# Kernel optimization log

Measured on AMD Instinct MI355X. Metric: run time of the kernel, lower is better.

Reference implementation:

```python
import jax, jax.numpy as jnp
import numpy as np

NUM_HEADS = 12
D = 768
HD = D // NUM_HEADS  # 64

def setup_inputs() -> dict:
    key = jax.random.key(0)
    ks = jax.random.split(key, 9)
    s = 0.02
    return {
        "x": jax.random.normal(ks[0], (4, 2048, D), dtype=jnp.float32),
        "QW_w": jax.random.normal(ks[1], (D, D), dtype=jnp.float32) * s,
        "QW_b": jax.random.normal(ks[2], (D,), dtype=jnp.float32) * s,
        "KW_w": jax.random.normal(ks[3], (D, D), dtype=jnp.float32) * s,
        "KW_b": jax.random.normal(ks[4], (D,), dtype=jnp.float32) * s,
        "VW_w": jax.random.normal(ks[5], (D, D), dtype=jnp.float32) * s,
        "VW_b": jax.random.normal(ks[6], (D,), dtype=jnp.float32) * s,
        "OW_w": jax.random.normal(ks[7], (D, D), dtype=jnp.float32) * s,
        "OW_b": jax.random.normal(ks[8], (D,), dtype=jnp.float32) * s,
    }

def reference(x, QW_w, QW_b, KW_w, KW_b, VW_w, VW_b, OW_w, OW_b):
    b, s, _ = x.shape
    # torch nn.Linear: y = x @ W.T + b
    def proj(w, bias):
        y = jnp.einsum('bsd,ed->bse', x, w) + bias
        return y.reshape(b, s, NUM_HEADS, HD).transpose(0, 2, 1, 3)  # [b,h,s,hd]
    q = proj(QW_w, QW_b)
    k = proj(KW_w, KW_b)
    v = proj(VW_w, VW_b)
    scores = jnp.einsum('bhqd,bhkd->bhqk', q, k) / jnp.sqrt(jnp.float32(HD))
    attn = jax.nn.softmax(scores, axis=-1)
    out = jnp.einsum('bhqk,bhkd->bhqd', attn, v)
    out = out.transpose(0, 2, 1, 3).reshape(b, s, NUM_HEADS * HD)
    return jnp.einsum('bsd,ed->bse', out, OW_w) + OW_b
```

## Files before the change

kernel.cpp:

```cpp
#include <hip/hip_runtime.h>
#include <hip/hip_bf16.h>

#define NH  12
#define HD  64
#define DIM 768
#define SEQ 2048
#define NB  4
#define MM  (NB*SEQ)
#define NKB (SEQ/64)

typedef short    v8s  __attribute__((ext_vector_type(8)));
typedef float    v4f  __attribute__((ext_vector_type(4)));
typedef float    v16f __attribute__((ext_vector_type(16)));
typedef unsigned v4u  __attribute__((ext_vector_type(4)));

#if __has_builtin(__builtin_amdgcn_exp2f)
#define EXP2(x) __builtin_amdgcn_exp2f(x)
#else
#define EXP2(x) __builtin_exp2f(x)
#endif

static __device__ __forceinline__ unsigned short f2b(float f) {
    unsigned int u = __float_as_uint(f);
    return (unsigned short)((u + 0x7FFFu + ((u >> 16) & 1u)) >> 16);
}
static __device__ __forceinline__ unsigned pk2bf(float lo, float hi) {
    return __builtin_amdgcn_perm(__float_as_uint(hi) + 0x8000u,
                                 __float_as_uint(lo) + 0x8000u, 0x07060302u);
}
static __device__ __forceinline__ void g2l16(const unsigned short* g, unsigned short* l) {
    __builtin_amdgcn_global_load_lds(
        (const __attribute__((address_space(1))) void*)g,
        (__attribute__((address_space(3))) void*)l, 16, 0, 0);
}

__global__ void cast_f32_bf16(const float* __restrict__ in,
                              unsigned short* __restrict__ out, int n4) {
    int i = blockIdx.x * blockDim.x + threadIdx.x;
    if (i < n4) {
        float4 v = reinterpret_cast<const float4*>(in)[i];
        ushort4 o;
        o.x = f2b(v.x); o.y = f2b(v.y); o.z = f2b(v.z); o.w = f2b(v.w);
        reinterpret_cast<ushort4*>(out)[i] = o;
    }
}

__global__ void cast4_f32_bf16(const float* __restrict__ i0, const float* __restrict__ i1,
                               const float* __restrict__ i2, const float* __restrict__ i3,
                               unsigned short* __restrict__ o0, unsigned short* __restrict__ o1,
                               unsigned short* __restrict__ o2, unsigned short* __restrict__ o3,
                               int n4) {
    int i = blockIdx.x * blockDim.x + threadIdx.x;
    if (i >= n4) return;
    const float* in; unsigned short* out;
    switch (blockIdx.y) {
        case 0: in = i0; out = o0; break;
        case 1: in = i1; out = o1; break;
        case 2: in = i2; out = o2; break;
        default: in = i3; out = o3; break;
    }
    float4 v = reinterpret_cast<const float4*>(in)[i];
    ushort4 o;
    o.x = f2b(v.x); o.y = f2b(v.y); o.z = f2b(v.z); o.w = f2b(v.w);
    reinterpret_cast<ushort4*>(out)[i] = o;
}

__global__ __launch_bounds__(256, 3) void gemm_qkv(
    const unsigned short* __restrict__ A,
    const unsigned short* __restrict__ Wq,
    const unsigned short* __restrict__ Wk,
    const unsigned short* __restrict__ Wv,
    const float* __restrict__ bq,
    const float* __restrict__ bk,
    const float* __restrict__ bvp,
    unsigned short* __restrict__ Qb,
    unsigned short* __restrict__ Kb,
    unsigned short* __restrict__ Vf)
{
    __shared__ __align__(16) unsigned short As[128 * 64];
    __shared__ __align__(16) unsigned short Bs[3][64 * 64];

    const int tid  = threadIdx.x;
    const int w    = tid >> 6, lane = tid & 63;
    const int quad = lane >> 4, l16 = lane & 15;
    const int wm   = w & 1,  wn = w >> 1;
    const int lane8 = lane >> 3, sc = lane & 7;
    const int m0   = blockIdx.x * 128;
    const int h    = blockIdx.y;
    const int n0   = h * 64;

    v4f acc[3][4][2];
    #pragma unroll
    for (int s = 0; s < 3; ++s)
        #pragma unroll
        for (int i = 0; i < 4; ++i)
            #pragma unroll
            for (int j = 0; j < 2; ++j)
                acc[s][i][j] = v4f{0.f, 0.f, 0.f, 0.f};

    for (int kb = 0; kb < DIM; kb += 64) {
        __syncthreads();
        #pragma unroll
        for (int t = 0; t < 4; ++t) {
            int r8 = w * 32 + t * 8;
            int r  = r8 + lane8;
            int gch = sc ^ (r & 7);
            g2l16(&A[(size_t)(m0 + r) * DIM + kb + gch * 8], &As[r8 * 64]);
        }
        #pragma unroll
        for (int u = 0; u < 6; ++u) {
            int G = w * 6 + u;
            int set = G >> 3, rg = G & 7;
            int row = rg * 8 + lane8;
            int gch = sc ^ (row & 7);
            const unsigned short* Wp = (set == 0) ? Wq : (set == 1) ? Wk : Wv;
            g2l16(&Wp[(size_t)(n0 + row) * DIM + kb + gch * 8], &Bs[set][rg * 8 * 64]);
        }
        __syncthreads();
        #pragma unroll
        for (int kk = 0; kk < 64; kk += 32) {
            int chb = kk >> 3;
            v8s a[4];
            #pragma unroll
            for (int i = 0; i < 4; ++i) {
                int m = wm * 64 + i * 16 + l16;
                a[i] = *reinterpret_cast<const v8s*>(
                    &As[m * 64 + (((chb + quad) ^ (m & 7)) << 3)]);
            }
            #pragma unroll
            for (int s = 0; s < 3; ++s) {
                v8s b[2];
                #pragma unroll
                for (int j = 0; j < 2; ++j) {
                    int n = wn * 32 + j * 16 + l16;
                    b[j] = *reinterpret_cast<const v8s*>(
                        &Bs[s][n * 64 + (((chb + quad) ^ (n & 7)) << 3)]);
                }
                #pragma unroll
                for (int i = 0; i < 4; ++i)
                    #pragma unroll
                    for (int j = 0; j < 2; ++j)
                        acc[s][i][j] = __builtin_amdgcn_mfma_f32_16x16x32_bf16(
                            a[i], b[j], acc[s][i][j], 0, 0, 0);
            }
        }
    }

    #pragma unroll
    for (int s = 0; s < 2; ++s) {
        unsigned short* out = s ? Kb : Qb;
        const float* bias   = s ? bk : bq;
        const float scale   = s ? 1.0f : 0.1803368801f;
        #pragma unroll
        for (int i = 0; i < 4; ++i) {
            #pragma unroll
            for (int j = 0; j < 2; ++j) {
                int hd = wn * 32 + j * 16 + l16;
                float bias_v = bias[n0 + hd];
                #pragma unroll
                for (int r = 0; r < 4; ++r) {
                    int gm = m0 + wm * 64 + i * 16 + quad * 4 + r;
                    int bb = gm >> 11, sq = gm & (SEQ - 1);
                    out[((size_t)(bb * NH + h) * SEQ + sq) * HD + hd] =
                        f2b((acc[s][i][j][r] + bias_v) * scale);
                }
            }
        }
    }
    #pragma unroll
    for (int i = 0; i < 4; ++i) {
        #pragma unroll
        for (int j = 0; j < 2; ++j) {
            int hd = wn * 32 + j * 16 + l16;
            int hb = hd >> 5, l31v = hd & 31;
            float bias_v = bvp[n0 + hd];
            int gm0 = m0 + wm * 64 + i * 16 + quad * 4;
            int bb = gm0 >> 11, sk = gm0 & (SEQ - 1);
            int kbi = sk >> 6;
            int halfv = quad >> 1, j0 = (quad & 1) * 4;
            ushort4 pkv;
            pkv.x = f2b(acc[2][i][j][0] + bias_v);
            pkv.y = f2b(acc[2][i][j][1] + bias_v);
            pkv.z = f2b(acc[2][i][j][2] + bias_v);
            pkv.w = f2b(acc[2][i][j][3] + bias_v);
            size_t frag = ((size_t)(bb * NH + h) * NKB + kbi) * 8 + hb * 4 + i;
            *reinterpret_cast<ushort4*>(
                &Vf[frag * 512 + (halfv * 32 + l31v) * 8 + j0]) = pkv;
        }
    }
}

__global__ __launch_bounds__(256, 3) void gemm_o(
    const unsigned short* __restrict__ A,
    const unsigned short* __restrict__ W,
    const float* __restrict__ bias,
    float* __restrict__ out)
{
    __shared__ __align__(16) unsigned short As[128 * 64];
    __shared__ __align__(16) unsigned short Bs[64 * 64];

    const int tid  = threadIdx.x;
    const int w    = tid >> 6, lane = tid & 63;
    const int quad = lane >> 4, l16 = lane & 15;
    const int wm   = w & 1,  wn = w >> 1;
    const int lane8 = lane >> 3, sc = lane & 7;
    const int m0  = blockIdx.x * 128;
    const int n0l = blockIdx.y * 64;

    v4f acc[4][2];
    #pragma unroll
    for (int i = 0; i < 4; ++i)
        #pragma unroll
        for (int j = 0; j < 2; ++j)
            acc[i][j] = v4f{0.f, 0.f, 0.f, 0.f};

    for (int kb = 0; kb < DIM; kb += 64) {
        __syncthreads();
        #pragma unroll
        for (int t = 0; t < 4; ++t) {
            int r8 = w * 32 + t * 8;
            int r  = r8 + lane8;
            int gch = sc ^ (r & 7);
            g2l16(&A[(size_t)(m0 + r) * DIM + kb + gch * 8], &As[r8 * 64]);
        }
        #pragma unroll
        for (int t = 0; t < 2; ++t) {
            int r8 = (w * 2 + t) * 8;
            int r  = r8 + lane8;
            int gch = sc ^ (r & 7);
            g2l16(&W[(size_t)(n0l + r) * DIM + kb + gch * 8], &Bs[r8 * 64]);
        }
        __syncthreads();
        #pragma unroll
        for (int kk = 0; kk < 64; kk += 32) {
            v8s a[4], b[2];
            int chb = kk >> 3;
            #pragma unroll
            for (int i = 0; i < 4; ++i) {
                int m = wm * 64 + i * 16 + l16;
                a[i] = *reinterpret_cast<const v8s*>(
                    &As[m * 64 + (((chb + quad) ^ (m & 7)) << 3)]);
            }
            #pragma unroll
            for (int j = 0; j < 2; ++j) {
                int n = wn * 32 + j * 16 + l16;
                b[j] = *reinterpret_cast<const v8s*>(
                    &Bs[n * 64 + (((chb + quad) ^ (n & 7)) << 3)]);
            }
            #pragma unroll
            for (int i = 0; i < 4; ++i)
                #pragma unroll
                for (int j = 0; j < 2; ++j)
                    acc[i][j] = __builtin_amdgcn_mfma_f32_16x16x32_bf16(a[i], b[j], acc[i][j], 0, 0, 0);
        }
    }

    #pragma unroll
    for (int i = 0; i < 4; ++i) {
        #pragma unroll
        for (int j = 0; j < 2; ++j) {
            int gn = n0l + wn * 32 + j * 16 + l16;
            float bias_v = bias[gn];
            #pragma unroll
            for (int r = 0; r < 4; ++r) {
                int gm = m0 + wm * 64 + i * 16 + quad * 4 + r;
                out[(size_t)gm * DIM + gn] = acc[i][j][r] + bias_v;
            }
        }
    }
}

__global__ __launch_bounds__(256, 3) void attn(
    const unsigned short* __restrict__ Q,
    const unsigned short* __restrict__ K,
    const unsigned short* __restrict__ Vf,
    unsigned short* __restrict__ ctx)
{
    __shared__ __align__(16) unsigned short Ks[2][64 * 64];

    const int tid  = threadIdx.x;
    const int w    = tid >> 6, lane = tid & 63;
    const int l31  = lane & 31, half = lane >> 5;
    const int lane8 = lane >> 3, sc = lane & 7;
    const int bh   = blockIdx.y;
    const int b    = bh / NH, h = bh % NH;
    const int q0   = blockIdx.x * 128 + w * 32;

    const unsigned short* Qp = Q  + ((size_t)bh * SEQ + q0) * HD;
    const unsigned short* Kp = K  + (size_t)bh * SEQ * HD;
    const unsigned short* Vh = Vf + (size_t)bh * NKB * 8 * 512 + lane * 8;

    v8s bq[4];
    #pragma unroll
    for (int c = 0; c < 4; ++c)
        bq[c] = *reinterpret_cast<const v8s*>(&Qp[l31 * HD + c * 16 + half * 8]);

    v8s va[2][4];
    #pragma unroll
    for (int hb = 0; hb < 2; ++hb)
        #pragma unroll
        for (int c = 0; c < 4; ++c)
            va[hb][c] = *reinterpret_cast<const v8s*>(&Vh[(hb * 4 + c) * 512]);

    v16f o0, o1, Z;
    #pragma unroll
    for (int i = 0; i < 16; ++i) { o0[i] = 0.f; o1[i] = 0.f; Z[i] = 0.f; }
    float li = 0.f;

    const int rx = l31 & 7;
    int rdoff[4];
    #pragma unroll
    for (int c = 0; c < 4; ++c)
        rdoff[c] = l31 * 64 + (((c * 2 + half) ^ rx) << 3);

    #define STAGE_K(kb_, buf_)                                                       \
        do {                                                                         \
            _Pragma("unroll")                                                        \
            for (int t = 0; t < 2; ++t) {                                            \
                int r8  = (t * 4 + w) * 8;                                           \
                int row = r8 + lane8;                                                \
                int gch = sc ^ (row & 7);                                            \
                g2l16(&Kp[(size_t)((kb_) + row) * HD + gch * 8], &Ks[buf_][r8 * 64]);\
            }                                                                        \
        } while (0)

    STAGE_K(0, 0);

    for (int it = 0; it < NKB; ++it) {
        const int buf = it & 1;
        __syncthreads();
        if (it + 1 < NKB) STAGE_K((it + 1) * 64, buf ^ 1);

        v16f s0, s1;
        {
            v8s ka00 = *reinterpret_cast<const v8s*>(&Ks[buf][rdoff[0]]);
            v8s ka10 = *reinterpret_cast<const v8s*>(&Ks[buf][rdoff[0] + 2048]);
            s0 = __builtin_amdgcn_mfma_f32_32x32x16_bf16(ka00, bq[0], Z, 0, 0, 0);
            s1 = __builtin_amdgcn_mfma_f32_32x32x16_bf16(ka10, bq[0], Z, 0, 0, 0);
            #pragma unroll
            for (int c = 1; c < 4; ++c) {
                v8s k0 = *reinterpret_cast<const v8s*>(&Ks[buf][rdoff[c]]);
                v8s k1 = *reinterpret_cast<const v8s*>(&Ks[buf][rdoff[c] + 2048]);
                s0 = __builtin_amdgcn_mfma_f32_32x32x16_bf16(k0, bq[c], s0, 0, 0, 0);
                s1 = __builtin_amdgcn_mfma_f32_32x32x16_bf16(k1, bq[c], s1, 0, 0, 0);
            }
        }

        unsigned pk[8][2];
        #pragma unroll
        for (int g = 0; g < 4; ++g) {
            float e0 = EXP2(s0[4*g+0]), e1 = EXP2(s0[4*g+1]);
            float e2 = EXP2(s0[4*g+2]), e3 = EXP2(s0[4*g+3]);
            li += (e0 + e1) + (e2 + e3);
            pk[g][0] = pk2bf(e0, e1);
            pk[g][1] = pk2bf(e2, e3);
            float f0 = EXP2(s1[4*g+0]), f1 = EXP2(s1[4*g+1]);
            float f2 = EXP2(s1[4*g+2]), f3 = EXP2(s1[4*g+3]);
            li += (f0 + f1) + (f2 + f3);
            pk[4+g][0] = pk2bf(f0, f1);
            pk[4+g][1] = pk2bf(f2, f3);
        }

        #pragma unroll
        for (int cp = 0; cp < 4; ++cp) {
            unsigned a0 = pk[2*cp][0],   a1 = pk[2*cp][1];
            unsigned b0 = pk[2*cp+1][0], b1 = pk[2*cp+1][1];
            unsigned u0 = half ? a0 : b0;
            unsigned u1 = half ? a1 : b1;
            unsigned x0 = __shfl_xor(u0, 32);
            unsigned x1 = __shfl_xor(u1, 32);
            v4u fw;
            fw.x = half ? x0 : a0;
            fw.y = half ? x1 : a1;
            fw.z = half ? b0 : x0;
            fw.w = half ? b1 : x1;
            v8s pf = __builtin_bit_cast(v8s, fw);
            o0 = __builtin_amdgcn_mfma_f32_32x32x16_bf16(va[0][cp], pf, o0, 0, 0, 0);
            o1 = __builtin_amdgcn_mfma_f32_32x32x16_bf16(va[1][cp], pf, o1, 0, 0, 0);
        }

        if (it + 1 < NKB) {
            const unsigned short* Vn = Vh + (size_t)(it + 1) * 8 * 512;
            #pragma unroll
            for (int hb = 0; hb < 2; ++hb)
                #pragma unroll
                for (int c = 0; c < 4; ++c)
                    va[hb][c] = *reinterpret_cast<const v8s*>(&Vn[(hb * 4 + c) * 512]);
        }
    }
    #undef STAGE_K

    float inv = 1.0f / (li + __shfl_xor(li, 32));

    const int q = q0 + l31;
    size_t base = ((size_t)(b * SEQ + q)) * DIM + h * HD;
    #pragma unroll
    for (int g = 0; g < 4; ++g) {
        int hd0 = 8 * g + 4 * half;
        uint2 u0, u1;
        u0.x = pk2bf(o0[4*g+0] * inv, o0[4*g+1] * inv);
        u0.y = pk2bf(o0[4*g+2] * inv, o0[4*g+3] * inv);
        u1.x = pk2bf(o1[4*g+0] * inv, o1[4*g+1] * inv);
        u1.y = pk2bf(o1[4*g+2] * inv, o1[4*g+3] * inv);
        *reinterpret_cast<uint2*>(&ctx[base + hd0])      = u0;
        *reinterpret_cast<uint2*>(&ctx[base + 32 + hd0]) = u1;
    }
}

extern "C" void kernel_launch(void* const* d_in, const int* in_sizes, int n_in,
                              void* d_out, int out_size, void* d_ws, size_t ws_size,
                              hipStream_t stream) {
    const float* x  = (const float*)d_in[0];
    const float* qw = (const float*)d_in[1]; const float* qb = (const float*)d_in[2];
    const float* kw = (const float*)d_in[3]; const float* kb = (const float*)d_in[4];
    const float* vw = (const float*)d_in[5]; const float* vb = (const float*)d_in[6];
    const float* ow = (const float*)d_in[7]; const float* ob = (const float*)d_in[8];
    float* out = (float*)d_out;

    char* ws = (char*)d_ws;
    size_t off = 0;
    auto alloc = [&](size_t bytes) -> unsigned short* {
        unsigned short* p = (unsigned short*)(ws + off);
        off += (bytes + 255) & ~(size_t)255;
        return p;
    };
    const size_t XB = (size_t)MM * DIM * 2;
    const size_t WB = (size_t)DIM * DIM * 2;
    const size_t QB = (size_t)NB * NH * SEQ * HD * 2;

    unsigned short* xb  = alloc(XB);
    unsigned short* wqb = alloc(WB);
    unsigned short* wkb = alloc(WB);
    unsigned short* wvb = alloc(WB);
    unsigned short* wob = alloc(WB);
    unsigned short* Qb  = alloc(QB);
    unsigned short* Kb  = alloc(QB);
    unsigned short* Vfb = alloc(QB);
    unsigned short* ctx = alloc(XB);

    const int n4x = MM * DIM / 4;
    const int n4w = DIM * DIM / 4;
    cast_f32_bf16<<<(n4x + 255) / 256, 256, 0, stream>>>(x, xb, n4x);
    cast4_f32_bf16<<<dim3((n4w + 255) / 256, 4), 256, 0, stream>>>(
        qw, kw, vw, ow, wqb, wkb, wvb, wob, n4w);

    gemm_qkv<<<dim3(MM / 128, NH), 256, 0, stream>>>(
        xb, wqb, wkb, wvb, qb, kb, vb, Qb, Kb, Vfb);

    attn<<<dim3(SEQ / 128, NB * NH), 256, 0, stream>>>(Qb, Kb, Vfb, ctx);

    gemm_o<<<dim3(MM / 128, DIM / 64), 256, 0, stream>>>(ctx, wob, ob, out);
}
```

Before: 208.7 us.

## Split attention key range across two wave groups and merge cast kernels

The attention kernel now launches 512 threads per block, with two groups of four waves each processing half of the key sequence for the same 128 queries. After the loop, group 1 writes its partial outputs and row sums to shared memory, and group 0 adds them, normalizes and stores. Because the kernel uses no running max, the two partial sums can simply be added. This doubles the waves per block and halves the serial key loop, at the cost of extra LDS traffic and a block-wide reduction. Separately, the x cast and the weight cast are fused into one launch to save kernel launch overhead.

```diff
diff --git a/kernel.cpp b/kernel.cpp
--- a/kernel.cpp
+++ b/kernel.cpp
@@ -8,6 +8,7 @@
 #define NB  4
 #define MM  (NB*SEQ)
 #define NKB (SEQ/64)
+#define NKB2 (NKB/2)
 
 typedef short    v8s  __attribute__((ext_vector_type(8)));
 typedef float    v4f  __attribute__((ext_vector_type(4)));
@@ -34,35 +35,28 @@
         (__attribute__((address_space(3))) void*)l, 16, 0, 0);
 }
 
-__global__ void cast_f32_bf16(const float* __restrict__ in,
-                              unsigned short* __restrict__ out, int n4) {
+__global__ void cast_all(const float* __restrict__ x,
+                         const float* __restrict__ qw, const float* __restrict__ kw,
+                         const float* __restrict__ vw, const float* __restrict__ ow,
+                         unsigned short* __restrict__ xb,
+                         unsigned short* __restrict__ wqb, unsigned short* __restrict__ wkb,
+                         unsigned short* __restrict__ wvb, unsigned short* __restrict__ wob) {
+    const int n4x = MM * DIM / 4, n4w = DIM * DIM / 4;
     int i = blockIdx.x * blockDim.x + threadIdx.x;
-    if (i < n4) {
-        float4 v = reinterpret_cast<const float4*>(in)[i];
-        ushort4 o;
-        o.x = f2b(v.x); o.y = f2b(v.y); o.z = f2b(v.z); o.w = f2b(v.w);
-        reinterpret_cast<ushort4*>(out)[i] = o;
-    }
-}
-
-__global__ void cast4_f32_bf16(const float* __restrict__ i0, const float* __restrict__ i1,
-                               const float* __restrict__ i2, const float* __restrict__ i3,
-                               unsigned short* __restrict__ o0, unsigned short* __restrict__ o1,
-                               unsigned short* __restrict__ o2, unsigned short* __restrict__ o3,
-                               int n4) {
-    int i = blockIdx.x * blockDim.x + threadIdx.x;
-    if (i >= n4) return;
-    const float* in; unsigned short* out;
-    switch (blockIdx.y) {
-        case 0: in = i0; out = o0; break;
-        case 1: in = i1; out = o1; break;
-        case 2: in = i2; out = o2; break;
-        default: in = i3; out = o3; break;
-    }
-    float4 v = reinterpret_cast<const float4*>(in)[i];
+    if (i >= n4x + 4 * n4w) return;
+    const float* in; unsigned short* out; int idx;
+    if (i < n4x) { in = x; out = xb; idx = i; }
+    else {
+        int j = i - n4x;
+        int s = j / n4w;
+        idx = j - s * n4w;
+        in  = (s == 0) ? qw : (s == 1) ? kw : (s == 2) ? vw : ow;
+        out = (s == 0) ? wqb : (s == 1) ? wkb : (s == 2) ? wvb : wob;
+    }
+    float4 v = reinterpret_cast<const float4*>(in)[idx];
     ushort4 o;
     o.x = f2b(v.x); o.y = f2b(v.y); o.z = f2b(v.z); o.w = f2b(v.w);
-    reinterpret_cast<ushort4*>(out)[i] = o;
+    reinterpret_cast<ushort4*>(out)[idx] = o;
 }
 
 __global__ __launch_bounds__(256, 3) void gemm_qkv(
@@ -270,21 +264,25 @@
     }
 }
 
-__global__ __launch_bounds__(256, 3) void attn(
+__global__ __launch_bounds__(512, 6) void attn(
     const unsigned short* __restrict__ Q,
     const unsigned short* __restrict__ K,
     const unsigned short* __restrict__ Vf,
     unsigned short* __restrict__ ctx)
 {
-    __shared__ __align__(16) unsigned short Ks[2][64 * 64];
+    __shared__ __align__(16) unsigned short Ks[2][2][64 * 64];
+    __shared__ float Ls[4][64];
 
     const int tid  = threadIdx.x;
     const int w    = tid >> 6, lane = tid & 63;
+    const int grp  = w >> 2, wl = w & 3;
     const int l31  = lane & 31, half = lane >> 5;
     const int lane8 = lane >> 3, sc = lane & 7;
     const int bh   = blockIdx.y;
     const int b    = bh / NH, h = bh % NH;
-    const int q0   = blockIdx.x * 128 + w * 32;
+    const int q0   = blockIdx.x * 128 + wl * 32;
+    const int kbase = grp * (SEQ / 2);
+    const int kbg   = grp * NKB2;
 
     const unsigned short* Qp = Q  + ((size_t)bh * SEQ + q0) * HD;
     const unsigned short* Kp = K  + (size_t)bh * SEQ * HD;
@@ -300,7 +298,8 @@
     for (int hb = 0; hb < 2; ++hb)
         #pragma unroll
         for (int c = 0; c < 4; ++c)
-            va[hb][c] = *reinterpret_cast<const v8s*>(&Vh[(hb * 4 + c) * 512]);
+            va[hb][c] = *reinterpret_cast<const v8s*>(
+                &Vh[(size_t)kbg * 4096 + (hb * 4 + c) * 512]);
 
     v16f o0, o1, Z;
     #pragma unroll
@@ -313,34 +312,36 @@
     for (int c = 0; c < 4; ++c)
         rdoff[c] = l31 * 64 + (((c * 2 + half) ^ rx) << 3);
 
-    #define STAGE_K(kb_, buf_)                                                       \
-        do {                                                                         \
-            _Pragma("unroll")                                                        \
-            for (int t = 0; t < 2; ++t) {                                            \
-                int r8  = (t * 4 + w) * 8;                                           \
-                int row = r8 + lane8;                                                \
-                int gch = sc ^ (row & 7);                                            \
-                g2l16(&Kp[(size_t)((kb_) + row) * HD + gch * 8], &Ks[buf_][r8 * 64]);\
-            }                                                                        \
+    #define STAGE_K(kb_, buf_)                                                        \
+        do {                                                                          \
+            _Pragma("unroll")                                                         \
+            for (int t = 0; t < 2; ++t) {                                             \
+                int r8  = (t * 4 + wl) * 8;                                           \
+                int row = r8 + lane8;                                                 \
+                int gch = sc ^ (row & 7);                                             \
+                g2l16(&Kp[(size_t)((kb_) + row) * HD + gch * 8],                      \
+                      &Ks[grp][buf_][r8 * 64]);                                       \
+            }                                                                         \
         } while (0)
 
-    STAGE_K(0, 0);
-
-    for (int it = 0; it < NKB; ++it) {
+    STAGE_K(kbase, 0);
+
+    for (int it = 0; it < NKB2; ++it) {
         const int buf = it & 1;
         __syncthreads();
-        if (it + 1 < NKB) STAGE_K((it + 1) * 64, buf ^ 1);
+        if (it + 1 < NKB2) STAGE_K(kbase + (it + 1) * 64, buf ^ 1);
 
         v16f s0, s1;
         {
-            v8s ka00 = *reinterpret_cast<const v8s*>(&Ks[buf][rdoff[0]]);
-            v8s ka10 = *reinterpret_cast<const v8s*>(&Ks[buf][rdoff[0] + 2048]);
+            const unsigned short* Kb_ = &Ks[grp][buf][0];
+            v8s ka00 = *reinterpret_cast<const v8s*>(&Kb_[rdoff[0]]);
+            v8s ka10 = *reinterpret_cast<const v8s*>(&Kb_[rdoff[0] + 2048]);
             s0 = __builtin_amdgcn_mfma_f32_32x32x16_bf16(ka00, bq[0], Z, 0, 0, 0);
             s1 = __builtin_amdgcn_mfma_f32_32x32x16_bf16(ka10, bq[0], Z, 0, 0, 0);
             #pragma unroll
             for (int c = 1; c < 4; ++c) {
-                v8s k0 = *reinterpret_cast<const v8s*>(&Ks[buf][rdoff[c]]);
-                v8s k1 = *reinterpret_cast<const v8s*>(&Ks[buf][rdoff[c] + 2048]);
+                v8s k0 = *reinterpret_cast<const v8s*>(&Kb_[rdoff[c]]);
+                v8s k1 = *reinterpret_cast<const v8s*>(&Kb_[rdoff[c] + 2048]);
                 s0 = __builtin_amdgcn_mfma_f32_32x32x16_bf16(k0, bq[c], s0, 0, 0, 0);
                 s1 = __builtin_amdgcn_mfma_f32_32x32x16_bf16(k1, bq[c], s1, 0, 0, 0);
             }
@@ -379,8 +380,8 @@
             o1 = __builtin_amdgcn_mfma_f32_32x32x16_bf16(va[1][cp], pf, o1, 0, 0, 0);
         }
 
-        if (it + 1 < NKB) {
-            const unsigned short* Vn = Vh + (size_t)(it + 1) * 8 * 512;
+        if (it + 1 < NKB2) {
+            const unsigned short* Vn = Vh + (size_t)(kbg + it + 1) * 4096;
             #pragma unroll
             for (int hb = 0; hb < 2; ++hb)
                 #pragma unroll
@@ -390,20 +391,38 @@
     }
     #undef STAGE_K
 
-    float inv = 1.0f / (li + __shfl_xor(li, 32));
-
-    const int q = q0 + l31;
-    size_t base = ((size_t)(b * SEQ + q)) * DIM + h * HD;
-    #pragma unroll
-    for (int g = 0; g < 4; ++g) {
-        int hd0 = 8 * g + 4 * half;
-        uint2 u0, u1;
-        u0.x = pk2bf(o0[4*g+0] * inv, o0[4*g+1] * inv);
-        u0.y = pk2bf(o0[4*g+2] * inv, o0[4*g+3] * inv);
-        u1.x = pk2bf(o1[4*g+0] * inv, o1[4*g+1] * inv);
-        u1.y = pk2bf(o1[4*g+2] * inv, o1[4*g+3] * inv);
-        *reinterpret_cast<uint2*>(&ctx[base + hd0])      = u0;
-        *reinterpret_cast<uint2*>(&ctx[base + 32 + hd0]) = u1;
+    float litot = li + __shfl_xor(li, 32);
+    float* Os = reinterpret_cast<float*>(&Ks[0][0][0]);
+    __syncthreads();
+    if (grp == 1) {
+        #pragma unroll
+        for (int r = 0; r < 16; ++r) {
+            Os[(wl * 32 + r)      * 64 + lane] = o0[r];
+            Os[(wl * 32 + 16 + r) * 64 + lane] = o1[r];
+        }
+        if (half == 0) Ls[wl][lane] = litot;
+    }
+    __syncthreads();
+    if (grp == 0) {
+        float inv = 1.0f / (litot + Ls[wl][l31]);
+        #pragma unroll
+        for (int r = 0; r < 16; ++r) {
+            o0[r] = (o0[r] + Os[(wl * 32 + r)      * 64 + lane]) * inv;
+            o1[r] = (o1[r] + Os[(wl * 32 + 16 + r) * 64 + lane]) * inv;
+        }
+        const int q = q0 + l31;
+        size_t base = ((size_t)(b * SEQ + q)) * DIM + h * HD;
+        #pragma unroll
+        for (int g = 0; g < 4; ++g) {
+            int hd0 = 8 * g + 4 * half;
+            uint2 u0, u1;
+            u0.x = pk2bf(o0[4*g+0], o0[4*g+1]);
+            u0.y = pk2bf(o0[4*g+2], o0[4*g+3]);
+            u1.x = pk2bf(o1[4*g+0], o1[4*g+1]);
+            u1.y = pk2bf(o1[4*g+2], o1[4*g+3]);
+            *reinterpret_cast<uint2*>(&ctx[base + hd0])      = u0;
+            *reinterpret_cast<uint2*>(&ctx[base + 32 + hd0]) = u1;
+        }
     }
 }
 
@@ -438,16 +457,15 @@
     unsigned short* Vfb = alloc(QB);
     unsigned short* ctx = alloc(XB);
 
-    const int n4x = MM * DIM / 4;
-    const int n4w = DIM * DIM / 4;
-    cast_f32_bf16<<<(n4x + 255) / 256, 256, 0, stream>>>(x, xb, n4x);
-    cast4_f32_bf16<<<dim3((n4w + 255) / 256, 4), 256, 0, stream>>>(
-        qw, kw, vw, ow, wqb, wkb, wvb, wob, n4w);
+    const int n4x = MM * DIM / 4, n4w = DIM * DIM / 4;
+    const int ncast = n4x + 4 * n4w;
+    cast_all<<<(ncast + 255) / 256, 256, 0, stream>>>(
+        x, qw, kw, vw, ow, xb, wqb, wkb, wvb, wob);
 
     gemm_qkv<<<dim3(MM / 128, NH), 256, 0, stream>>>(
         xb, wqb, wkb, wvb, qb, kb, vb, Qb, Kb, Vfb);
 
-    attn<<<dim3(SEQ / 128, NB * NH), 256, 0, stream>>>(Qb, Kb, Vfb, ctx);
+    attn<<<dim3(SEQ / 128, NB * NH), 512, 0, stream>>>(Qb, Kb, Vfb, ctx);
 
     gemm_o<<<dim3(MM / 128, DIM / 64), 256, 0, stream>>>(ctx, wob, ob, out);
 }
```

After: 602.3 us. 2.89x slower.
